# Performance work log

Measured on AMD Instinct MI355X. Metric: run time of the kernel, lower is better.

## Reference

```python
import jax, jax.numpy as jnp
import numpy as np

BN_EPS = 1e-5
CURVE_LENGTH = 8

def _gumbel_st(logits):
    # straight-through gumbel-softmax (no gumbel noise, temperature=1), over last dim
    y = jax.nn.softmax(logits, axis=-1)
    ind = jnp.argmax(y, axis=-1)
    y_hard = jax.nn.one_hot(ind, logits.shape[-1], dtype=y.dtype)
    return jax.lax.stop_gradient(y_hard - y) + y

def _crossover(cur_vec, nb):
    # cur_vec: (B, c), nb: (B, c, k) -> clamp(1 + cosine, 0, 1), detached
    cur_vec = jax.lax.stop_gradient(cur_vec)
    nb = jax.lax.stop_gradient(nb)
    dot = jnp.einsum('bc,bck->bk', cur_vec, nb)
    n1 = jnp.linalg.norm(cur_vec, axis=1, keepdims=True)        # (B, 1)
    n2 = jnp.linalg.norm(nb, axis=1)                            # (B, k)
    cos = dot / jnp.maximum(n1 * n2, 1e-8)
    return jnp.clip(1.0 + cos, 0.0, 1.0)

def walk_forward(x, adj, cur, agent_w, agent_gamma, agent_beta, agent_mean, agent_var,
                 mom_w, mom_gamma, mom_beta, mom_mean, mom_var):
    bn, c, tot = x.shape
    k = adj.shape[-1]
    cn = cur.shape[1]
    flatten_x = jnp.transpose(x, (0, 2, 1)).reshape(bn * tot, c)
    offset = (jnp.arange(bn, dtype=adj.dtype) * tot)[:, None, None]
    tmp_adj = (adj + offset).reshape(bn * tot, k)
    flatten_cur = (cur + offset).reshape(-1)                    # (bn*cn,)
    inv_agent = agent_gamma / jnp.sqrt(agent_var + BN_EPS)      # (1,)
    inv_mom = mom_gamma / jnp.sqrt(mom_var + BN_EPS)            # (2,)
    rows = jnp.arange(bn * cn)
    curves = []
    pre_feature = cur_feature = cur_feature_cos = pre_feature_cos = None
    for step in range(CURVE_LENGTH):
        if step == 0:
            pre_feature = jnp.transpose(flatten_x[flatten_cur].reshape(bn, cn, c, 1), (0, 2, 1, 3))  # (bn,c,cn,1)
        else:
            cat1 = jnp.concatenate([cur_feature[..., 0], pre_feature[..., 0]], axis=1)  # (bn,2c,cn)
            mlog = jnp.einsum('bcn,oc->bon', cat1, mom_w)
            mlog = (mlog - mom_mean[None, :, None]) * inv_mom[None, :, None] + mom_beta[None, :, None]
            att = jax.nn.softmax(mlog, axis=1).reshape(bn, 1, cn, 2)  # faithful to torch .view
            cat2 = jnp.concatenate([cur_feature, pre_feature], axis=-1)  # (bn,c,cn,2)
            pre_feature = jnp.sum(cat2 * att, axis=-1, keepdims=True)    # (bn,c,cn,1)
            pre_feature_cos = jnp.transpose(pre_feature, (0, 2, 1, 3)).reshape(bn * cn, c)
        pick_idx = tmp_adj[flatten_cur]                                  # (bn*cn, k)
        pv_flat = flatten_x[pick_idx.reshape(-1)].reshape(bn * cn, k, c)
        pv_cos = jnp.transpose(pv_flat, (0, 2, 1))                       # (bn*cn, c, k)
        pick_values = jnp.transpose(pv_flat.reshape(bn, cn, k, c), (0, 3, 1, 2))  # (bn,c,cn,k)
        cat3 = jnp.concatenate([pick_values, jnp.broadcast_to(pre_feature, pick_values.shape)], axis=1)  # (bn,2c,cn,k)
        logits = jnp.einsum('bcnk,c->bnk', cat3, agent_w)[:, None]       # conv2d 1x1 -> (bn,1,cn,k)
        logits = (logits - agent_mean[0]) * inv_agent[0] + agent_beta[0]
        if step != 0:
            d = _crossover(cur_feature_cos - pre_feature_cos, pv_cos - cur_feature_cos[..., None])
            logits = logits * d.reshape(bn, cn, k)[:, None]
        sel = _gumbel_st(logits)                                         # (bn,1,cn,k)
        cur_feature = jnp.sum(pick_values * sel, axis=-1, keepdims=True)  # (bn,c,cn,1)
        cur_feature_cos = jnp.transpose(cur_feature, (0, 2, 1, 3)).reshape(bn * cn, c)
        cur_idx = jnp.argmax(sel, axis=-1).reshape(-1)                   # (bn*cn,)
        flatten_cur = pick_idx[rows, cur_idx]
        curves.append(cur_feature)
    return jnp.concatenate(curves, axis=-1)  # (bn, c, cn, curve_length)

def setup_inputs() -> dict:
    key = jax.random.key(0)
    ks = jax.random.split(key, 12)
    bn, c, tot, k, cn = 16, 64, 8192, 20, 512
    xyz = jax.random.normal(ks[0], (bn, 3, tot), dtype=jnp.float32)
    x = jax.random.normal(ks[1], (bn, c, tot), dtype=jnp.float32)
    adj = jax.random.randint(ks[2], (bn, tot, k), 0, tot)
    cur = jax.random.randint(ks[3], (bn, cn, 1), 0, tot)
    sc = 1.0 / np.sqrt(2 * c)
    agent_w = jax.random.normal(ks[4], (2 * c,), dtype=jnp.float32) * sc
    mom_w = jax.random.normal(ks[5], (2, 2 * c), dtype=jnp.float32) * sc
    agent_gamma = 1.0 + 0.1 * jax.random.normal(ks[6], (1,), dtype=jnp.float32)
    agent_beta = 0.1 * jax.random.normal(ks[7], (1,), dtype=jnp.float32)
    agent_mean = 0.1 * jax.random.normal(ks[8], (1,), dtype=jnp.float32)
    agent_var = jax.random.uniform(ks[9], (1,), minval=0.5, maxval=1.5, dtype=jnp.float32)
    mom_gamma = 1.0 + 0.1 * jax.random.normal(ks[10], (2,), dtype=jnp.float32)
    mom_beta = 0.1 * jax.random.normal(ks[11], (2,), dtype=jnp.float32)
    mom_mean = 0.1 * jax.random.normal(jax.random.fold_in(key, 101), (2,), dtype=jnp.float32)
    mom_var = jax.random.uniform(jax.random.fold_in(key, 102), (2,), minval=0.5, maxval=1.5, dtype=jnp.float32)
    return {"xyz": xyz, "x": x, "adj": adj, "cur": cur,
            "agent_w": agent_w, "agent_gamma": agent_gamma, "agent_beta": agent_beta,
            "agent_mean": agent_mean, "agent_var": agent_var,
            "mom_w": mom_w, "mom_gamma": mom_gamma, "mom_beta": mom_beta,
            "mom_mean": mom_mean, "mom_var": mom_var}

def reference(xyz, x, adj, cur, agent_w, agent_gamma, agent_beta, agent_mean, agent_var,
              mom_w, mom_gamma, mom_beta, mom_mean, mom_var):
    # xyz is accepted (as in the torch forward) but never used: the original code
    # calls `xyz.transpose(1, 2).contiguous` without invoking it.
    return walk_forward(x, adj, cur, agent_w, agent_gamma, agent_beta, agent_mean,
                        agent_var, mom_w, mom_gamma, mom_beta, mom_mean, mom_var)
```

## Files before the change

kernel.cpp:

```cpp
#include <hip/hip_runtime.h>
#include <cmath>

#define BN 16
#define CDIM 64
#define TOT 8192
#define KNB 20
#define CN 512
#define NSTEPS 8
#define WPB 16
#define BPB 32
#define WSTRIDE 577
#define LINE 32
#define MAGIC 0x5A17ECE1u
#define POISON 0xAAAAAAAAu

typedef float vf4 __attribute__((ext_vector_type(4)));

__device__ __forceinline__ float dot4(float a, float b, float c, float d,
                                      float wa, float wb, float wc, float wd) {
  return a * wa + b * wb + c * wc + d * wd;
}

template <int CTRL>
__device__ __forceinline__ float dpp_add(float v) {
  int o = __builtin_amdgcn_update_dpp(0, __float_as_int(v), CTRL, 0xF, 0xF, true);
  return v + __int_as_float(o);
}

__device__ __forceinline__ float gred16(float v) {
  v = dpp_add<0xB1>(v);
  v = dpp_add<0x4E>(v);
  v = dpp_add<0x141>(v);
  v = dpp_add<0x140>(v);
  return v;
}

__global__ __launch_bounds__(256, 2) void walk_kernel(
    const float* __restrict__ x, const int* __restrict__ adj, const int* __restrict__ cur,
    const float* __restrict__ agent_w, const float* __restrict__ agent_gamma,
    const float* __restrict__ agent_beta, const float* __restrict__ agent_mean,
    const float* __restrict__ agent_var, const float* __restrict__ mom_w,
    const float* __restrict__ mom_gamma, const float* __restrict__ mom_beta,
    const float* __restrict__ mom_mean, const float* __restrict__ mom_var,
    float* __restrict__ xt, float* __restrict__ pa,
    float* __restrict__ out, float* __restrict__ sbuf,
    unsigned int* __restrict__ pflag) {
  __shared__ float lds_out[WPB * WSTRIDE];
  const int tid  = threadIdx.x;
  const int lane = tid & 63;
  const int wv   = tid >> 6;
  const int g    = lane >> 4;
  const int L    = lane & 15;
  const int b     = (blockIdx.x & 7) + (((blockIdx.x >> 8) & 1) << 3);
  const int chunk = (blockIdx.x >> 3) & 31;
  const int w     = wv * 4 + g;
  const int n     = chunk * WPB + w;
  const int c0    = L << 2;
  const int mbase = (n << 2) & 1023;
  const int moff  = (n >= 256) ? 1 : 0;

  {
    float (*tile)[65] = (float (*)[65])lds_out;
#pragma unroll 1
    for (int i = 0; i < 4; ++i) {
      const int t0 = ((chunk << 2) + i) << 6;
#pragma unroll
      for (int k = 0; k < 4; ++k) {
        int fid = tid + k * 256;
        int cc = fid >> 4, qt = (fid & 15) << 2;
        float4 vv = *(const float4*)(x + ((size_t)b * CDIM + cc) * TOT + t0 + qt);
        tile[cc][qt + 0] = vv.x; tile[cc][qt + 1] = vv.y;
        tile[cc][qt + 2] = vv.z; tile[cc][qt + 3] = vv.w;
      }
      __syncthreads();
#pragma unroll
      for (int k = 0; k < 4; ++k) {
        int fid = tid + k * 256;
        int tt = fid >> 4, qc = (fid & 15) << 2;
        vf4 vv = {tile[qc + 0][tt], tile[qc + 1][tt], tile[qc + 2][tt], tile[qc + 3][tt]};
        float* dst = xt + ((size_t)b * TOT + t0 + tt) * CDIM + qc;
        asm volatile("global_store_dwordx4 %0, %1, off sc0 sc1" :: "v"(dst), "v"(vv) : "memory");
      }
      if (tid < 64) {
        const int tt = tid;
        float q[16];
#pragma unroll
        for (int l = 0; l < 16; ++l)
          q[l] = dot4(tile[4 * l][tt], tile[4 * l + 1][tt],
                      tile[4 * l + 2][tt], tile[4 * l + 3][tt],
                      agent_w[4 * l], agent_w[4 * l + 1],
                      agent_w[4 * l + 2], agent_w[4 * l + 3]);
        float sA = (q[0] + q[1]) + (q[2] + q[3]);
        float sB = (q[4] + q[5]) + (q[6] + q[7]);
        float sC = (q[8] + q[9]) + (q[10] + q[11]);
        float sD = (q[12] + q[13]) + (q[14] + q[15]);
        __hip_atomic_store(pa + (size_t)b * TOT + t0 + tt, (sA + sB) + (sC + sD),
                           __ATOMIC_RELAXED, __HIP_MEMORY_SCOPE_AGENT);
      }
      __syncthreads();
    }
    asm volatile("s_waitcnt vmcnt(0)" ::: "memory");
    __builtin_amdgcn_s_barrier();
    if (tid == 0)
      __hip_atomic_store(pflag + ((size_t)b * BPB + chunk) * LINE, MAGIC,
                         __ATOMIC_RELAXED, __HIP_MEMORY_SCOPE_AGENT);
    if (tid < BPB) {
      const unsigned int* f = pflag + ((size_t)b * BPB + tid) * LINE;
      while (__hip_atomic_load(f, __ATOMIC_RELAXED, __HIP_MEMORY_SCOPE_AGENT) != MAGIC)
        __builtin_amdgcn_s_sleep(2);
    }
    __builtin_amdgcn_s_barrier();
    asm volatile("" ::: "memory");
  }

  const vf4 aw2  = *(const vf4*)(agent_w + 64 + c0);
  const vf4 mw0a = *(const vf4*)(mom_w + c0);
  const vf4 mw0b = *(const vf4*)(mom_w + 64 + c0);
  const vf4 mw1a = *(const vf4*)(mom_w + 128 + c0);
  const vf4 mw1b = *(const vf4*)(mom_w + 192 + c0);
  const float amean  = agent_mean[0];
  const float abeta  = agent_beta[0];
  const float ainv   = agent_gamma[0] / sqrtf(agent_var[0] + 1e-5f);
  const float m0mean = mom_mean[0], m1mean = mom_mean[1];
  const float m0inv  = mom_gamma[0] / sqrtf(mom_var[0] + 1e-5f);
  const float m1inv  = mom_gamma[1] / sqrtf(mom_var[1] + 1e-5f);
  const float m0beta = mom_beta[0], m1beta = mom_beta[1];

  const float* xb   = xt + (size_t)b * TOT * CDIM;
  const float* pab  = pa + (size_t)b * TOT;
  const int*   adjb = adj + (size_t)b * TOT * KNB;
  float*       lout = lds_out + w * WSTRIDE;

  int t = cur[b * CN + n];
  vf4 pf = *(const vf4*)(xb + (size_t)t * CDIM + c0);
  vf4 cf = pf;
  vf4 u  = (vf4){0.f, 0.f, 0.f, 0.f};
  float A0v = 0.f, A1v = 0.f;

  int   idx[KNB];
  vf4   nv[KNB];
  float pav[KNB];
  float sq[KNB];
  {
    const int4* arow = (const int4*)(adjb + (size_t)t * KNB);
    int4 q0 = arow[0], q1 = arow[1], q2 = arow[2], q3 = arow[3], q4 = arow[4];
    int tmp[KNB] = {q0.x, q0.y, q0.z, q0.w, q1.x, q1.y, q1.z, q1.w,
                    q2.x, q2.y, q2.z, q2.w, q3.x, q3.y, q3.z, q3.w,
                    q4.x, q4.y, q4.z, q4.w};
#pragma unroll
    for (int j = 0; j < KNB; ++j) idx[j] = tmp[j];
#pragma unroll
    for (int j = 0; j < KNB; ++j) {
      nv[j]  = *(const vf4*)(xb + (size_t)idx[j] * CDIM + c0);
      pav[j] = pab[idx[j]];
    }
  }

#pragma unroll 1
  for (int s = 0; s < NSTEPS; ++s) {
    float n1 = 0.f;
    if (s > 0) {
      pf.x = A0v * cf.x + A1v * pf.x;
      pf.y = A0v * cf.y + A1v * pf.y;
      pf.z = A0v * cf.z + A1v * pf.z;
      pf.w = A0v * cf.w + A1v * pf.w;
      u.x = cf.x - pf.x; u.y = cf.y - pf.y; u.z = cf.z - pf.z; u.w = cf.w - pf.w;
      n1 = sqrtf(gred16(u.x * u.x + u.y * u.y + u.z * u.z + u.w * u.w));
    }
    float pw = gred16(pf.x * aw2.x + pf.y * aw2.y + pf.z * aw2.z + pf.w * aw2.w);

    float bestp = -3.4e38f;
    int   bestt = 0;
    vf4   bestv = (vf4){0.f, 0.f, 0.f, 0.f};
#pragma unroll
    for (int j = 0; j < KNB; ++j) {
      const vf4 v = nv[j];
      float logit = (pav[j] + pw - amean) * ainv + abeta;
      float p;
      if (s > 0) {
        float tx = v.x - cf.x, ty = v.y - cf.y, tz = v.z - cf.z, tw = v.w - cf.w;
        float su = tx * u.x + ty * u.y + tz * u.z + tw * u.w;
        su = gred16(su);
        float den  = fmaxf(n1 * sq[j], 1e-8f);
        float cosv = su * __builtin_amdgcn_rcpf(den);
        float dfac = fminf(fmaxf(1.0f + cosv, 0.0f), 1.0f);
        p = logit * dfac;
      } else {
        p = logit;
      }
      if (p > bestp) { bestp = p; bestt = idx[j]; bestv = v; }
    }
    cf = bestv;
    t  = bestt;
    lout[(c0 + 0) * 9 + s] = cf.x;
    lout[(c0 + 1) * 9 + s] = cf.y;
    lout[(c0 + 2) * 9 + s] = cf.z;
    lout[(c0 + 3) * 9 + s] = cf.w;

    if (s < NSTEPS - 1) {
      float p0 = cf.x * mw0a.x + cf.y * mw0a.y + cf.z * mw0a.z + cf.w * mw0a.w +
                 pf.x * mw0b.x + pf.y * mw0b.y + pf.z * mw0b.z + pf.w * mw0b.w;
      float p1 = cf.x * mw1a.x + cf.y * mw1a.y + cf.z * mw1a.z + cf.w * mw1a.w +
                 pf.x * mw1b.x + pf.y * mw1b.y + pf.z * mw1b.z + pf.w * mw1b.w;
      p0 = gred16(p0);
      p1 = gred16(p1);
      float mlog0 = (p0 - m0mean) * m0inv + m0beta;
      float mlog1 = (p1 - m1mean) * m1inv + m1beta;
      float mx = fmaxf(mlog0, mlog1);
      float e0 = expf(mlog0 - mx), e1 = expf(mlog1 - mx);
      float sinv = 1.0f / (e0 + e1);
      float* sb = sbuf + ((size_t)(b * NSTEPS + s + 1) << 10);
      if (L == 0) {
        unsigned long long pk =
            (unsigned long long)__float_as_uint(e0 * sinv) |
            ((unsigned long long)__float_as_uint(e1 * sinv) << 32);
        __hip_atomic_store((unsigned long long*)sb + n, pk,
                           __ATOMIC_RELAXED, __HIP_MEMORY_SCOPE_AGENT);
      }
      const int4* arow = (const int4*)(adjb + (size_t)t * KNB);
      int4 q0 = arow[0], q1 = arow[1], q2 = arow[2], q3 = arow[3], q4 = arow[4];
      int tmp[KNB] = {q0.x, q0.y, q0.z, q0.w, q1.x, q1.y, q1.z, q1.w,
                      q2.x, q2.y, q2.z, q2.w, q3.x, q3.y, q3.z, q3.w,
                      q4.x, q4.y, q4.z, q4.w};
#pragma unroll
      for (int j = 0; j < KNB; ++j) idx[j] = tmp[j];
#pragma unroll
      for (int j = 0; j < KNB; ++j) {
        nv[j]  = *(const vf4*)(xb + (size_t)idx[j] * CDIM + c0);
        pav[j] = pab[idx[j]];
      }
#pragma unroll
      for (int j = 0; j < KNB; ++j) {
        const vf4 v = nv[j];
        float tx = v.x - cf.x, ty = v.y - cf.y, tz = v.z - cf.z, tw = v.w - cf.w;
        float sn = tx * tx + ty * ty + tz * tz + tw * tw;
        sq[j] = sqrtf(gred16(sn));
      }
      {
        const unsigned* sbw = (const unsigned*)sb;
        const unsigned* q0p = sbw + mbase + moff;
        const unsigned* q2p = q0p + 2;
        unsigned w0, w2;
        for (;;) {
          w0 = __hip_atomic_load(q0p, __ATOMIC_RELAXED, __HIP_MEMORY_SCOPE_AGENT);
          w2 = __hip_atomic_load(q2p, __ATOMIC_RELAXED, __HIP_MEMORY_SCOPE_AGENT);
          if (w0 != POISON && w2 != POISON) break;
          __builtin_amdgcn_s_sleep(1);
        }
        A0v = __uint_as_float(w0);
        A1v = __uint_as_float(w2);
      }
      asm volatile("" ::: "memory");
    }
  }

#pragma unroll
  for (int e = 0; e < 4; ++e) {
    const float* src = lout + (c0 + e) * 9;
    float4 w0 = make_float4(src[0], src[1], src[2], src[3]);
    float4 w1 = make_float4(src[4], src[5], src[6], src[7]);
    float* op = out + (((size_t)(b * CDIM + c0 + e) * CN) + n) * NSTEPS;
    *(float4*)(op)     = w0;
    *(float4*)(op + 4) = w1;
  }
}

extern "C" void kernel_launch(void* const* d_in, const int* in_sizes, int n_in,
                              void* d_out, int out_size, void* d_ws, size_t ws_size,
                              hipStream_t stream) {
  (void)in_sizes; (void)n_in; (void)out_size; (void)ws_size;
  const float* x          = (const float*)d_in[1];
  const int*   adj        = (const int*)d_in[2];
  const int*   cur        = (const int*)d_in[3];
  const float* agent_w    = (const float*)d_in[4];
  const float* agent_gamma= (const float*)d_in[5];
  const float* agent_beta = (const float*)d_in[6];
  const float* agent_mean = (const float*)d_in[7];
  const float* agent_var  = (const float*)d_in[8];
  const float* mom_w      = (const float*)d_in[9];
  const float* mom_gamma  = (const float*)d_in[10];
  const float* mom_beta   = (const float*)d_in[11];
  const float* mom_mean   = (const float*)d_in[12];
  const float* mom_var    = (const float*)d_in[13];
  float* out = (float*)d_out;

  char* ws = (char*)d_ws;
  const size_t xt_bytes   = (size_t)BN * TOT * CDIM * sizeof(float);
  const size_t sbuf_bytes = (size_t)BN * NSTEPS * 2 * CN * sizeof(float);
  const size_t pa_bytes   = (size_t)BN * TOT * sizeof(float);
  float*        xt    = (float*)ws;
  float*        sbuf  = (float*)(ws + xt_bytes);
  float*        pab   = (float*)(ws + xt_bytes + sbuf_bytes);
  unsigned int* pflag = (unsigned int*)(ws + xt_bytes + sbuf_bytes + pa_bytes);

  walk_kernel<<<BN * BPB, 256, 0, stream>>>(x, adj, cur, agent_w, agent_gamma, agent_beta,
                                            agent_mean, agent_var, mom_w, mom_gamma, mom_beta,
                                            mom_mean, mom_var, xt, pab, out, sbuf, pflag);
}
```

Baseline: 162.5 us.

## Split transpose into separate prep kernel and halve neighbors per half-wave

Moves the x transpose and agent-weight dot product out of the walk kernel into a dedicated prep kernel, which removes the in-kernel flag-based grid barrier and its spin waits. The walk kernel now gives each walker 32 lanes instead of 16. Each 16-lane group scores 10 of the 20 neighbors, and the two groups merge their argmax with a cross-half shuffle. This halves per-thread register arrays, so occupancy can rise to 4 blocks and twice as many blocks are launched. The cost is an extra kernel launch and a shuffle-based reduction each step, and the tie-break order must match the original first-max semantics.

Result: slower. 178.6 us (+9.9%).

```diff
diff --git a/kernel.cpp b/kernel.cpp
--- a/kernel.cpp
+++ b/kernel.cpp
@@ -7,11 +7,10 @@
 #define KNB 20
 #define CN 512
 #define NSTEPS 8
-#define WPB 16
-#define BPB 32
+#define WPB 8
+#define BPB 64
+#define NNB 10
 #define WSTRIDE 577
-#define LINE 32
-#define MAGIC 0x5A17ECE1u
 #define POISON 0xAAAAAAAAu
 
 typedef float vf4 __attribute__((ext_vector_type(4)));
@@ -35,83 +34,58 @@
   return v;
 }
 
-__global__ __launch_bounds__(256, 2) void walk_kernel(
-    const float* __restrict__ x, const int* __restrict__ adj, const int* __restrict__ cur,
+__global__ __launch_bounds__(256) void prep_kernel(
+    const float* __restrict__ x, const float* __restrict__ agent_w,
+    float* __restrict__ xt, float* __restrict__ pa) {
+  __shared__ float tile[64][65];
+  const int tid = threadIdx.x;
+  const int bI  = blockIdx.x;
+  const int b   = (bI & 7) | (((bI >> 10) & 1) << 3);
+  const int t0  = ((bI >> 3) & 127) << 6;
+  const vf4 aw  = *(const vf4*)(agent_w + ((tid & 15) << 2));
+#pragma unroll
+  for (int k = 0; k < 4; ++k) {
+    int fid = tid + (k << 8);
+    int cc = fid >> 4, qt = (fid & 15) << 2;
+    float4 vv = *(const float4*)(x + ((size_t)b * CDIM + cc) * TOT + t0 + qt);
+    tile[cc][qt + 0] = vv.x; tile[cc][qt + 1] = vv.y;
+    tile[cc][qt + 2] = vv.z; tile[cc][qt + 3] = vv.w;
+  }
+  __syncthreads();
+#pragma unroll
+  for (int k = 0; k < 4; ++k) {
+    int fid = tid + (k << 8);
+    int tt = fid >> 4, qc = (fid & 15) << 2;
+    vf4 vv = {tile[qc + 0][tt], tile[qc + 1][tt], tile[qc + 2][tt], tile[qc + 3][tt]};
+    *(vf4*)(xt + ((size_t)b * TOT + t0 + tt) * CDIM + qc) = vv;
+    float part = gred16(dot4(vv.x, vv.y, vv.z, vv.w, aw.x, aw.y, aw.z, aw.w));
+    if ((tid & 15) == 0) pa[(size_t)b * TOT + t0 + tt] = part;
+  }
+}
+
+__global__ __launch_bounds__(256, 4) void walk_kernel(
+    const int* __restrict__ adj, const int* __restrict__ cur,
     const float* __restrict__ agent_w, const float* __restrict__ agent_gamma,
     const float* __restrict__ agent_beta, const float* __restrict__ agent_mean,
     const float* __restrict__ agent_var, const float* __restrict__ mom_w,
     const float* __restrict__ mom_gamma, const float* __restrict__ mom_beta,
     const float* __restrict__ mom_mean, const float* __restrict__ mom_var,
-    float* __restrict__ xt, float* __restrict__ pa,
-    float* __restrict__ out, float* __restrict__ sbuf,
-    unsigned int* __restrict__ pflag) {
+    const float* __restrict__ xt, const float* __restrict__ pa,
+    float* __restrict__ out, float* __restrict__ sbuf) {
   __shared__ float lds_out[WPB * WSTRIDE];
   const int tid  = threadIdx.x;
   const int lane = tid & 63;
   const int wv   = tid >> 6;
-  const int g    = lane >> 4;
+  const int half = lane >> 5;
+  const int g2   = (lane >> 4) & 1;
   const int L    = lane & 15;
-  const int b     = (blockIdx.x & 7) + (((blockIdx.x >> 8) & 1) << 3);
-  const int chunk = (blockIdx.x >> 3) & 31;
-  const int w     = wv * 4 + g;
+  const int w    = wv * 2 + half;
+  const int b     = (blockIdx.x & 7) | (((blockIdx.x >> 9) & 1) << 3);
+  const int chunk = (blockIdx.x >> 3) & 63;
   const int n     = chunk * WPB + w;
   const int c0    = L << 2;
   const int mbase = (n << 2) & 1023;
   const int moff  = (n >= 256) ? 1 : 0;
-
-  {
-    float (*tile)[65] = (float (*)[65])lds_out;
-#pragma unroll 1
-    for (int i = 0; i < 4; ++i) {
-      const int t0 = ((chunk << 2) + i) << 6;
-#pragma unroll
-      for (int k = 0; k < 4; ++k) {
-        int fid = tid + k * 256;
-        int cc = fid >> 4, qt = (fid & 15) << 2;
-        float4 vv = *(const float4*)(x + ((size_t)b * CDIM + cc) * TOT + t0 + qt);
-        tile[cc][qt + 0] = vv.x; tile[cc][qt + 1] = vv.y;
-        tile[cc][qt + 2] = vv.z; tile[cc][qt + 3] = vv.w;
-      }
-      __syncthreads();
-#pragma unroll
-      for (int k = 0; k < 4; ++k) {
-        int fid = tid + k * 256;
-        int tt = fid >> 4, qc = (fid & 15) << 2;
-        vf4 vv = {tile[qc + 0][tt], tile[qc + 1][tt], tile[qc + 2][tt], tile[qc + 3][tt]};
-        float* dst = xt + ((size_t)b * TOT + t0 + tt) * CDIM + qc;
-        asm volatile("global_store_dwordx4 %0, %1, off sc0 sc1" :: "v"(dst), "v"(vv) : "memory");
-      }
-      if (tid < 64) {
-        const int tt = tid;
-        float q[16];
-#pragma unroll
-        for (int l = 0; l < 16; ++l)
-          q[l] = dot4(tile[4 * l][tt], tile[4 * l + 1][tt],
-                      tile[4 * l + 2][tt], tile[4 * l + 3][tt],
-                      agent_w[4 * l], agent_w[4 * l + 1],
-                      agent_w[4 * l + 2], agent_w[4 * l + 3]);
-        float sA = (q[0] + q[1]) + (q[2] + q[3]);
-        float sB = (q[4] + q[5]) + (q[6] + q[7]);
-        float sC = (q[8] + q[9]) + (q[10] + q[11]);
-        float sD = (q[12] + q[13]) + (q[14] + q[15]);
-        __hip_atomic_store(pa + (size_t)b * TOT + t0 + tt, (sA + sB) + (sC + sD),
-                           __ATOMIC_RELAXED, __HIP_MEMORY_SCOPE_AGENT);
-      }
-      __syncthreads();
-    }
-    asm volatile("s_waitcnt vmcnt(0)" ::: "memory");
-    __builtin_amdgcn_s_barrier();
-    if (tid == 0)
-      __hip_atomic_store(pflag + ((size_t)b * BPB + chunk) * LINE, MAGIC,
-                         __ATOMIC_RELAXED, __HIP_MEMORY_SCOPE_AGENT);
-    if (tid < BPB) {
-      const unsigned int* f = pflag + ((size_t)b * BPB + tid) * LINE;
-      while (__hip_atomic_load(f, __ATOMIC_RELAXED, __HIP_MEMORY_SCOPE_AGENT) != MAGIC)
-        __builtin_amdgcn_s_sleep(2);
-    }
-    __builtin_amdgcn_s_barrier();
-    asm volatile("" ::: "memory");
-  }
 
   const vf4 aw2  = *(const vf4*)(agent_w + 64 + c0);
   const vf4 mw0a = *(const vf4*)(mom_w + c0);
@@ -137,20 +111,17 @@
   vf4 u  = (vf4){0.f, 0.f, 0.f, 0.f};
   float A0v = 0.f, A1v = 0.f;
 
-  int   idx[KNB];
-  vf4   nv[KNB];
-  float pav[KNB];
-  float sq[KNB];
+  int   idx[NNB];
+  vf4   nv[NNB];
+  float pav[NNB];
+  float sq[NNB];
   {
-    const int4* arow = (const int4*)(adjb + (size_t)t * KNB);
-    int4 q0 = arow[0], q1 = arow[1], q2 = arow[2], q3 = arow[3], q4 = arow[4];
-    int tmp[KNB] = {q0.x, q0.y, q0.z, q0.w, q1.x, q1.y, q1.z, q1.w,
-                    q2.x, q2.y, q2.z, q2.w, q3.x, q3.y, q3.z, q3.w,
-                    q4.x, q4.y, q4.z, q4.w};
-#pragma unroll
-    for (int j = 0; j < KNB; ++j) idx[j] = tmp[j];
-#pragma unroll
-    for (int j = 0; j < KNB; ++j) {
+    const int2* ar = (const int2*)(adjb + (size_t)t * KNB + g2 * NNB);
+    int2 a0 = ar[0], a1 = ar[1], a2 = ar[2], a3 = ar[3], a4 = ar[4];
+    idx[0] = a0.x; idx[1] = a0.y; idx[2] = a1.x; idx[3] = a1.y; idx[4] = a2.x;
+    idx[5] = a2.y; idx[6] = a3.x; idx[7] = a3.y; idx[8] = a4.x; idx[9] = a4.y;
+#pragma unroll
+    for (int j = 0; j < NNB; ++j) {
       nv[j]  = *(const vf4*)(xb + (size_t)idx[j] * CDIM + c0);
       pav[j] = pab[idx[j]];
     }
@@ -173,7 +144,7 @@
     int   bestt = 0;
     vf4   bestv = (vf4){0.f, 0.f, 0.f, 0.f};
 #pragma unroll
-    for (int j = 0; j < KNB; ++j) {
+    for (int j = 0; j < NNB; ++j) {
       const vf4 v = nv[j];
       float logit = (pav[j] + pw - amean) * ainv + abeta;
       float p;
@@ -190,12 +161,24 @@
       }
       if (p > bestp) { bestp = p; bestt = idx[j]; bestv = v; }
     }
+    {
+      float op = __shfl_xor(bestp, 16, 32);
+      int   ot = __shfl_xor(bestt, 16, 32);
+      float ox = __shfl_xor(bestv.x, 16, 32);
+      float oy = __shfl_xor(bestv.y, 16, 32);
+      float oz = __shfl_xor(bestv.z, 16, 32);
+      float ow = __shfl_xor(bestv.w, 16, 32);
+      bool take = g2 ? !(bestp > op) : (op > bestp);
+      if (take) { bestt = ot; bestv.x = ox; bestv.y = oy; bestv.z = oz; bestv.w = ow; }
+    }
     cf = bestv;
     t  = bestt;
-    lout[(c0 + 0) * 9 + s] = cf.x;
-    lout[(c0 + 1) * 9 + s] = cf.y;
-    lout[(c0 + 2) * 9 + s] = cf.z;
-    lout[(c0 + 3) * 9 + s] = cf.w;
+    if (g2 == 0) {
+      lout[(c0 + 0) * 9 + s] = cf.x;
+      lout[(c0 + 1) * 9 + s] = cf.y;
+      lout[(c0 + 2) * 9 + s] = cf.z;
+      lout[(c0 + 3) * 9 + s] = cf.w;
+    }
 
     if (s < NSTEPS - 1) {
       float p0 = cf.x * mw0a.x + cf.y * mw0a.y + cf.z * mw0a.z + cf.w * mw0a.w +
@@ -210,27 +193,24 @@
       float e0 = expf(mlog0 - mx), e1 = expf(mlog1 - mx);
       float sinv = 1.0f / (e0 + e1);
       float* sb = sbuf + ((size_t)(b * NSTEPS + s + 1) << 10);
-      if (L == 0) {
+      if (L == 0 && g2 == 0) {
         unsigned long long pk =
             (unsigned long long)__float_as_uint(e0 * sinv) |
             ((unsigned long long)__float_as_uint(e1 * sinv) << 32);
         __hip_atomic_store((unsigned long long*)sb + n, pk,
                            __ATOMIC_RELAXED, __HIP_MEMORY_SCOPE_AGENT);
       }
-      const int4* arow = (const int4*)(adjb + (size_t)t * KNB);
-      int4 q0 = arow[0], q1 = arow[1], q2 = arow[2], q3 = arow[3], q4 = arow[4];
-      int tmp[KNB] = {q0.x, q0.y, q0.z, q0.w, q1.x, q1.y, q1.z, q1.w,
-                      q2.x, q2.y, q2.z, q2.w, q3.x, q3.y, q3.z, q3.w,
-                      q4.x, q4.y, q4.z, q4.w};
-#pragma unroll
-      for (int j = 0; j < KNB; ++j) idx[j] = tmp[j];
-#pragma unroll
-      for (int j = 0; j < KNB; ++j) {
+      const int2* ar = (const int2*)(adjb + (size_t)t * KNB + g2 * NNB);
+      int2 a0 = ar[0], a1 = ar[1], a2 = ar[2], a3 = ar[3], a4 = ar[4];
+      idx[0] = a0.x; idx[1] = a0.y; idx[2] = a1.x; idx[3] = a1.y; idx[4] = a2.x;
+      idx[5] = a2.y; idx[6] = a3.x; idx[7] = a3.y; idx[8] = a4.x; idx[9] = a4.y;
+#pragma unroll
+      for (int j = 0; j < NNB; ++j) {
         nv[j]  = *(const vf4*)(xb + (size_t)idx[j] * CDIM + c0);
         pav[j] = pab[idx[j]];
       }
 #pragma unroll
-      for (int j = 0; j < KNB; ++j) {
+      for (int j = 0; j < NNB; ++j) {
         const vf4 v = nv[j];
         float tx = v.x - cf.x, ty = v.y - cf.y, tz = v.z - cf.z, tw = v.w - cf.w;
         float sn = tx * tx + ty * ty + tz * tz + tw * tw;
@@ -255,11 +235,12 @@
   }
 
 #pragma unroll
-  for (int e = 0; e < 4; ++e) {
-    const float* src = lout + (c0 + e) * 9;
+  for (int e = 0; e < 2; ++e) {
+    const int ee = (g2 << 1) + e;
+    const float* src = lout + (c0 + ee) * 9;
     float4 w0 = make_float4(src[0], src[1], src[2], src[3]);
     float4 w1 = make_float4(src[4], src[5], src[6], src[7]);
-    float* op = out + (((size_t)(b * CDIM + c0 + e) * CN) + n) * NSTEPS;
+    float* op = out + (((size_t)(b * CDIM + c0 + ee) * CN) + n) * NSTEPS;
     *(float4*)(op)     = w0;
     *(float4*)(op + 4) = w1;
   }
@@ -287,13 +268,13 @@
   char* ws = (char*)d_ws;
   const size_t xt_bytes   = (size_t)BN * TOT * CDIM * sizeof(float);
   const size_t sbuf_bytes = (size_t)BN * NSTEPS * 2 * CN * sizeof(float);
-  const size_t pa_bytes   = (size_t)BN * TOT * sizeof(float);
-  float*        xt    = (float*)ws;
-  float*        sbuf  = (float*)(ws + xt_bytes);
-  float*        pab   = (float*)(ws + xt_bytes + sbuf_bytes);
-  unsigned int* pflag = (unsigned int*)(ws + xt_bytes + sbuf_bytes + pa_bytes);
-
-  walk_kernel<<<BN * BPB, 256, 0, stream>>>(x, adj, cur, agent_w, agent_gamma, agent_beta,
-                                            agent_mean, agent_var, mom_w, mom_gamma, mom_beta,
-                                            mom_mean, mom_var, xt, pab, out, sbuf, pflag);
-}
+  float* xt   = (float*)ws;
+  float* sbuf = (float*)(ws + xt_bytes);
+  float* pab  = (float*)(ws + xt_bytes + sbuf_bytes);
+
+  prep_kernel<<<2048, 256, 0, stream>>>(x, agent_w, xt, pab);
+  walk_kernel<<<BN * BPB, 256, 0, stream>>>(adj, cur, agent_w, agent_gamma, agent_beta,
+                                            agent_mean, agent_var, mom_w, mom_gamma,
+                                            mom_beta, mom_mean, mom_var,
+                                            xt, pab, out, sbuf);
+}
```
